# Performance work log

Hardware: AMD Instinct MI355X
Metric: run time of the kernel (lower is better)

Reference implementation:

```python
import jax, jax.numpy as jnp
import numpy as np

B, S, D, H, P = 4, 512, 4096, 32, 10
HD = D // H          # 128
R = 16               # lora rank
HID = 11008          # multiple_of-rounded 2/3 * 4*dim
MAXSEQ = 512
EPS = 1e-5
SCALE = 1.0 / (HD ** 0.5)


def setup_inputs() -> dict:
    key = jax.random.key(0)
    ks = jax.random.split(key, 40)
    rn = lambda k, shp, s=0.02: (jax.random.normal(k, shp, jnp.float32) * s)
    inp = {}
    inp['x'] = jax.random.normal(ks[0], (B, S, D), jnp.float32)
    inp['prompt'] = jax.random.normal(ks[1], (B, P, D), jnp.float32)
    causal = jnp.where(jnp.arange(S)[:, None] >= jnp.arange(S)[None, :], 0.0, -1e9)
    inp['mask'] = causal[None, None].astype(jnp.float32)
    inp['cache_k'] = jnp.zeros((B, MAXSEQ, H, HD), jnp.float32)
    inp['cache_v'] = jnp.zeros((B, MAXSEQ, H, HD), jnp.float32)
    freqs = 1.0 / (10000.0 ** (np.arange(0, HD, 2)[: HD // 2].astype(np.float32) / HD))
    ang = np.outer(np.arange(S), freqs).astype(np.float32)  # [S, HD//2]
    inp['freqs_cos'] = jnp.asarray(np.cos(ang))
    inp['freqs_sin'] = jnp.asarray(np.sin(ang))
    # attention weights (torch Linear layout: [out, in])
    inp['wq_w'] = rn(ks[2], (D, D)); inp['wq_b'] = jnp.zeros((D,), jnp.float32)
    inp['wk_w'] = rn(ks[3], (D, D))
    inp['wv_w'] = rn(ks[4], (D, D))
    inp['wo_w'] = rn(ks[5], (D, D)); inp['wo_b'] = jnp.zeros((D,), jnp.float32)
    inp['lq1'] = rn(ks[6], (R, D)); inp['lq2'] = rn(ks[7], (D, R), 0.01)
    inp['lk1'] = rn(ks[8], (R, D)); inp['lk2'] = rn(ks[9], (D, R), 0.01)
    inp['lv1'] = rn(ks[10], (R, D)); inp['lv2'] = rn(ks[11], (D, R), 0.01)
    inp['lo1'] = rn(ks[12], (R, D)); inp['lo2'] = rn(ks[13], (D, R), 0.01)
    inp['gate'] = rn(ks[14], (1, H, 1, 1), 0.5)
    inp['new_gate'] = jnp.ones((1, 1, 1, 1), jnp.float32)
    inp['attn_norm_w'] = jnp.ones((D,), jnp.float32)
    inp['ffn_norm_w'] = jnp.ones((D,), jnp.float32)
    inp['w1_w'] = rn(ks[15], (HID, D)); inp['w1_b'] = jnp.zeros((HID,), jnp.float32)
    inp['w2_w'] = rn(ks[16], (D, HID)); inp['w2_b'] = jnp.zeros((D,), jnp.float32)
    inp['w3_w'] = rn(ks[17], (HID, D)); inp['w3_b'] = jnp.zeros((HID,), jnp.float32)
    inp['fl1a'] = rn(ks[18], (R, D)); inp['fl1b'] = rn(ks[19], (HID, R), 0.01)
    inp['fl2a'] = rn(ks[20], (R, HID)); inp['fl2b'] = rn(ks[21], (D, R), 0.01)
    inp['fl3a'] = rn(ks[22], (R, D)); inp['fl3b'] = rn(ks[23], (HID, R), 0.01)
    inp['start_pos'] = 0
    return inp


def _rms(v, w):
    return v * jax.lax.rsqrt(jnp.mean(v * v, axis=-1, keepdims=True) + EPS) * w


def _rope(t, cos, sin):
    # t: [B,S,H,HD]; treat last dim as interleaved (real, imag) pairs
    t2 = t.reshape(*t.shape[:-1], HD // 2, 2)
    a, b = t2[..., 0], t2[..., 1]
    c = cos[None, :, None, :]
    s = sin[None, :, None, :]
    return jnp.stack([a * c - b * s, a * s + b * c], axis=-1).reshape(t.shape)


def reference(x, prompt, mask, cache_k, cache_v, freqs_cos, freqs_sin,
              wq_w, wq_b, wk_w, wv_w, wo_w, wo_b,
              lq1, lq2, lk1, lk2, lv1, lv2, lo1, lo2,
              gate, new_gate, attn_norm_w, ffn_norm_w,
              w1_w, w1_b, w2_w, w2_b, w3_w, w3_b,
              fl1a, fl1b, fl2a, fl2b, fl3a, fl3b, start_pos):
    bsz, seqlen, _ = x.shape
    # --- attention sub-layer ---
    h = _rms(x, attn_norm_w)
    xq = h @ wq_w.T + wq_b + (h @ lq1.T) @ lq2.T
    xk = h @ wk_w.T + (h @ lk1.T) @ lk2.T
    xv = h @ wv_w.T + (h @ lv1.T) @ lv2.T
    xq = xq.reshape(bsz, seqlen, H, HD)
    xk = xk.reshape(bsz, seqlen, H, HD)
    xv = xv.reshape(bsz, seqlen, H, HD)
    xq = _rope(xq, freqs_cos, freqs_sin)
    xk = _rope(xk, freqs_cos, freqs_sin)
    # KV-cache update (functional)
    cache_k = jax.lax.dynamic_update_slice(cache_k, xk, (0, start_pos, 0, 0))
    cache_v = jax.lax.dynamic_update_slice(cache_v, xv, (0, start_pos, 0, 0))
    keys = cache_k[:, : start_pos + seqlen].transpose(0, 2, 1, 3)    # b h k d
    values = cache_v[:, : start_pos + seqlen].transpose(0, 2, 1, 3)  # b h k d
    q = xq.transpose(0, 2, 1, 3)                                     # b h q d
    scores = jnp.einsum('bhqd,bhkd->bhqk', q, keys) * SCALE
    scores = jax.nn.softmax(scores + mask, axis=-1)
    out = jnp.einsum('bhqk,bhkd->bhqd', scores, values)
    # gated prompt attention branch (no LoRA on prompt k/v, matching source)
    pk = (prompt @ wk_w.T).reshape(bsz, P, H, HD).transpose(0, 2, 1, 3)
    pv = (prompt @ wv_w.T).reshape(bsz, P, H, HD).transpose(0, 2, 1, 3)
    ps = jnp.einsum('bhqd,bhpd->bhqp', q, pk) * SCALE
    ps = jnp.tanh(gate) * new_gate * jax.nn.softmax(ps, axis=-1)
    out = out + jnp.einsum('bhqp,bhpd->bhqd', ps, pv)
    out = out.transpose(0, 2, 1, 3).reshape(bsz, seqlen, D)
    attn = out @ wo_w.T + wo_b + (out @ lo1.T) @ lo2.T
    h2 = x + attn
    # --- SwiGLU FFN with LoRA ---
    g = _rms(h2, ffn_norm_w)
    a1 = g @ w1_w.T + w1_b + (g @ fl1a.T) @ fl1b.T
    a3 = g @ w3_w.T + w3_b + (g @ fl3a.T) @ fl3b.T
    o = jax.nn.silu(a1) * a3
    ffn = o @ w2_w.T + w2_b + (o @ fl2a.T) @ fl2b.T
    return h2 + ffn
```

## Files before the change

### kernel.cpp

```cpp
#include <hip/hip_runtime.h>

typedef int    i32x4 __attribute__((ext_vector_type(4)));
typedef float  f32x4 __attribute__((ext_vector_type(4)));
typedef __bf16 bf16x8 __attribute__((ext_vector_type(8)));
typedef unsigned int u32;
typedef unsigned short u16;

#define SCALEF 0.08838834764831845f
#define EPSF 1e-5f

__device__ __forceinline__ u16 f2bf(float f) {
  u32 u = __float_as_uint(f);
  u32 r = (u + 0x7fffu + ((u >> 16) & 1u)) >> 16;
  return (u16)r;
}
__device__ __forceinline__ float bf2f(u16 h) { return __uint_as_float(((u32)h) << 16); }
__device__ __forceinline__ u32 pack2(float a, float b) {
  return (u32)f2bf(a) | ((u32)f2bf(b) << 16);
}

__device__ __forceinline__ void gload16(const u16* g, u16* l) {
  __builtin_amdgcn_global_load_lds(
      (const __attribute__((address_space(1))) void*)g,
      (__attribute__((address_space(3))) void*)l, 16, 0, 0);
}


#define G_PHASE(MFMAS) \
  __builtin_amdgcn_s_barrier(); \
  __builtin_amdgcn_s_setprio(1); \
  MFMAS \
  __builtin_amdgcn_s_setprio(0); \
  __builtin_amdgcn_s_barrier();

#define MM(KH, MB, MI, NI) \
  acc[(MB)+(MI)][NI] = __builtin_amdgcn_mfma_f32_16x16x32_bf16( \
      aa[KH][MI], bb[KH][NI], acc[(MB)+(MI)][NI], 0, 0, 0);

#define MM8(MB, NI) MM(0,MB,0,NI) MM(0,MB,1,NI) MM(0,MB,2,NI) MM(0,MB,3,NI) \
                    MM(1,MB,0,NI) MM(1,MB,1,NI) MM(1,MB,2,NI) MM(1,MB,3,NI)

#define RDA4(P, KH, MG) \
  aa[KH][0] = *(const bf16x8*)(pAk[P][KH] + ((MG)*4+0)*2048); \
  aa[KH][1] = *(const bf16x8*)(pAk[P][KH] + ((MG)*4+1)*2048); \
  aa[KH][2] = *(const bf16x8*)(pAk[P][KH] + ((MG)*4+2)*2048); \
  aa[KH][3] = *(const bf16x8*)(pAk[P][KH] + ((MG)*4+3)*2048);

#define RDB1(P, NI) \
  bb[0][NI] = *(const bf16x8*)(pBk[P][0] + (NI)*2048); \
  bb[1][NI] = *(const bf16x8*)(pBk[P][1] + (NI)*2048);

#define STAGE_A(P, HH, KT) \
  gload16(sA + ((HH)*2+0)*lda64 + (long)(KT)*64, (u16*)(lds + (P)*BUFB + (HH)*16384 + w*1024)); \
  gload16(sA + ((HH)*2+1)*lda64 + (long)(KT)*64, (u16*)(lds + (P)*BUFB + (HH)*16384 + 8192 + w*1024));

#define STAGE_B(P, HH, KT) \
  gload16(sB + ((HH)*2+0)*ldb64 + (long)(KT)*64, (u16*)(lds + (P)*BUFB + 32768 + (HH)*16384 + w*1024)); \
  gload16(sB + ((HH)*2+1)*ldb64 + (long)(KT)*64, (u16*)(lds + (P)*BUFB + 32768 + (HH)*16384 + 8192 + w*1024));

#define GEMM_TILE(P, PN, TA, TC) \
  RDA4(P,0,0) RDA4(P,1,0) \
  RDB1(P,0) RDB1(P,1) \
  STAGE_A(PN, 1, TA) \
  G_PHASE(MM8(0,0) MM8(0,1)) \
  RDB1(P,2) RDB1(P,3) \
  G_PHASE(MM8(0,2) MM8(0,3)) \
  RDA4(P,0,1) RDA4(P,1,1) \
  STAGE_B(P, 0, TC) \
  G_PHASE(MM8(4,0) MM8(4,1)) \
  STAGE_B(P, 1, TC) \
  STAGE_A(P, 0, TC) \
  asm volatile("s_waitcnt vmcnt(6)" ::: "memory"); \
  G_PHASE(MM8(4,2) MM8(4,3))

#define GEMM_TILE2(P, PN, TA, TC) \
  RDA4(P,0,0) RDA4(P,1,0) \
  RDB1(P,0) RDB1(P,1) \
  STAGE_A(PN, 0, TA) \
  STAGE_A(PN, 1, TA) \
  G_PHASE(MM8(0,0) MM8(0,1)) \
  RDA4(P,0,1) RDA4(P,1,1) \
  STAGE_B(P, 0, TC) \
  asm volatile("s_waitcnt vmcnt(2)" ::: "memory"); \
  G_PHASE(MM8(4,0) MM8(4,1))

template<int NF, int OUT>
__global__ __launch_bounds__(512, 2) void gemm256(
    const u16* __restrict__ A, const u16* __restrict__ B, void* Cv,
    const float* __restrict__ bias, const float* __restrict__ bias2, int nsplit,
    const float* res, int K, int lda, int ldb, int ldc)
{
  extern __shared__ char lds[];
  constexpr int BN = NF * 64;
  constexpr int BUFB = (NF == 4) ? 65536 : 49152;

  const int tid = threadIdx.x, w = tid >> 6, l = tid & 63;
  const int wm = w >> 2, wn = w & 3;

  const int gy = gridDim.y;
  const int nwg = gridDim.x * gy;
  const int orig = blockIdx.y * gridDim.x + blockIdx.x;
  const int q = nwg >> 3, r = nwg & 7;
  const int xcd = orig & 7, sidx = orig >> 3;
  const int wg = (xcd < r ? xcd * (q + 1) : r * (q + 1) + (xcd - r) * q) + sidx;
  const int bx = wg / gy, by = wg % gy;
  const long row0 = (long)by * 256, col0 = (long)bx * BN;

  const int g4 = l >> 4, h8 = l & 7, r16 = l & 15;
  const int cs0 = ((g4 ^ h8) << 4);
  const int cs1 = cs0 ^ 64;
  const char* pAk[2][2];
  const char* pBk[2][2];
  {
    const int aoff = wm * 16384 + r16 * 128;
    const int boff = 32768 + ((NF == 4) ? ((wn >> 1) * 16384 + (wn & 1) * 8192)
                                        : (wn * 4096)) + r16 * 128;
    pAk[0][0] = lds + aoff + cs0;        pAk[0][1] = lds + aoff + cs1;
    pAk[1][0] = pAk[0][0] + BUFB;        pAk[1][1] = pAk[0][1] + BUFB;
    pBk[0][0] = lds + boff + cs0;        pBk[0][1] = lds + boff + cs1;
    pBk[1][0] = pBk[0][0] + BUFB;        pBk[1][1] = pBk[0][1] + BUFB;
  }

  const long ldaL = lda, ldbL = ldb;
  const long lda64 = ldaL * 64, ldb64 = ldbL * 64;
  const int srow = w * 8 + (l >> 3);
  const int scol = ((h8 ^ (l >> 3)) << 3);
  const u16* sA = A + (row0 + srow) * ldaL + scol;
  const u16* sB = B + (col0 + srow) * ldbL + scol;

  f32x4 acc[8][4];
  #pragma unroll
  for (int m = 0; m < 8; m++)
    #pragma unroll
    for (int n = 0; n < 4; n++)
      #pragma unroll
      for (int j = 0; j < 4; j++) acc[m][n][j] = 0.f;

  bf16x8 aa[2][4], bb[2][4];

  const int NT = K >> 6;
  if constexpr (NF == 4) {
    STAGE_A(0,0,0) STAGE_A(0,1,0) STAGE_B(0,0,0) STAGE_B(0,1,0)
    STAGE_B(1,0,1) STAGE_B(1,1,1) STAGE_A(1,0,1)
    asm volatile("s_waitcnt vmcnt(6)" ::: "memory");
    __builtin_amdgcn_s_barrier();
    for (int t = 0; t < NT; t += 2) {
      const int ta = (t + 1 < NT) ? t + 1 : NT - 1;
      const int tb = (t + 2 < NT) ? t + 2 : NT - 1;
      const int tc = (t + 3 < NT) ? t + 3 : NT - 1;
      GEMM_TILE(0, 1, ta, tb)
      GEMM_TILE(1, 0, tb, tc)
    }
  } else {
    STAGE_A(0,0,0) STAGE_A(0,1,0) STAGE_B(0,0,0)
    STAGE_B(1,0,1)
    asm volatile("s_waitcnt vmcnt(2)" ::: "memory");
    __builtin_amdgcn_s_barrier();
    for (int t = 0; t < NT; t += 2) {
      const int ta = (t + 1 < NT) ? t + 1 : NT - 1;
      const int tb = (t + 2 < NT) ? t + 2 : NT - 1;
      const int tc = (t + 3 < NT) ? t + 3 : NT - 1;
      GEMM_TILE2(0, 1, ta, tb)
      GEMM_TILE2(1, 0, tb, tc)
    }
  }

  const int cc = l & 15, cr = (l >> 4) * 4;
  #pragma unroll
  for (int mf = 0; mf < 8; mf++) {
    const long rrow = row0 + wm * 128 + mf * 16 + cr;
    if constexpr (OUT == 2) {
      #pragma unroll
      for (int nfp = 0; nfp < NF / 2; nfp++) {
        const long outc = (col0 >> 1) + wn * 32 + nfp * 16 + cc;
        const float b1 = bias[outc], b3 = bias2[outc];
        #pragma unroll
        for (int j = 0; j < 4; j++) {
          const float v1 = acc[mf][2 * nfp][j] + b1;
          const float v3 = acc[mf][2 * nfp + 1][j] + b3;
          const float o = v1 / (1.f + __expf(-v1)) * v3;
          ((u16*)Cv)[(rrow + j) * ldc + outc] = f2bf(o);
        }
      }
    } else {
      #pragma unroll
      for (int nf = 0; nf < 4 && nf < NF; nf++) {
        const long ccol = col0 + wn * (NF * 16) + nf * 16 + cc;
        float bb2 = 0.f;
        if (bias) bb2 = (ccol < nsplit) ? bias[ccol] : (bias2 ? bias2[ccol - nsplit] : 0.f);
        #pragma unroll
        for (int j = 0; j < 4; j++) {
          const long off = (rrow + j) * ldc + ccol;
          float v = acc[mf][nf][j] + bb2;
          if constexpr (OUT == 0) {
            if (res) v += res[off];
            ((float*)Cv)[off] = v;
          } else {
            ((u16*)Cv)[off] = f2bf(v);
          }
        }
      }
    }
  }
}

template<int EPI>
__global__ __launch_bounds__(256) void gemm_bt(
    const u16* __restrict__ A, const u16* __restrict__ B,
    float* __restrict__ Cf, u16* __restrict__ Cbf, const float* __restrict__ Cadd,
    int K, int lda, int ldb, int ldc, float scale,
    long sAb, long sBb, int cInnerN, long cSO, long cSI, int causal, int kvar)
{
  if (causal && blockIdx.x > blockIdx.y) return;
  const int Keff = kvar ? (int)(blockIdx.y + 1) * 128 : K;

  __shared__ u16 As[128*32] __attribute__((aligned(16)));
  __shared__ u16 Bs[128*32] __attribute__((aligned(16)));
  const int tid  = threadIdx.x;
  const int wave = tid >> 6, lane = tid & 63;
  const int wm = wave >> 1, wn = wave & 1;
  const int z = blockIdx.z;
  const u16* Ab = A + (long)z * sAb;
  const u16* Bb = B + (long)z * sBb;
  const long cb = (long)(z / cInnerN) * cSO + (long)(z % cInnerN) * cSI;

  const int sr = lane >> 2;
  const int sc = (lane & 3) * 8;
  const int c0 = wave * 2, c1 = wave * 2 + 1;
  const u16* gA0 = Ab + (long)(blockIdx.y * 128 + c0 * 16 + sr) * lda + sc;
  const u16* gA1 = Ab + (long)(blockIdx.y * 128 + c1 * 16 + sr) * lda + sc;
  const u16* gB0 = Bb + (long)(blockIdx.x * 128 + c0 * 16 + sr) * ldb + sc;
  const u16* gB1 = Bb + (long)(blockIdx.x * 128 + c1 * 16 + sr) * ldb + sc;
  u16* lA0 = &As[c0 * 512]; u16* lA1 = &As[c1 * 512];
  u16* lB0 = &Bs[c0 * 512]; u16* lB1 = &Bs[c1 * 512];

  f32x4 acc[4][4];
  #pragma unroll
  for (int m = 0; m < 4; m++)
    #pragma unroll
    for (int n = 0; n < 4; n++)
      #pragma unroll
      for (int j = 0; j < 4; j++) acc[m][n][j] = 0.f;

  const int fr  = lane & 15;
  const int fg8 = (lane >> 4) * 8;

  for (int k0 = 0; k0 < Keff; k0 += 32) {
    __syncthreads();
    gload16(gA0 + k0, lA0);
    gload16(gA1 + k0, lA1);
    gload16(gB0 + k0, lB0);
    gload16(gB1 + k0, lB1);
    __syncthreads();

    bf16x8 af[4], bfr[4];
    #pragma unroll
    for (int m = 0; m < 4; m++)
      af[m] = *(const bf16x8*)&As[(wm * 64 + m * 16 + fr) * 32 + fg8];
    #pragma unroll
    for (int n = 0; n < 4; n++)
      bfr[n] = *(const bf16x8*)&Bs[(wn * 64 + n * 16 + fr) * 32 + fg8];

    #pragma unroll
    for (int m = 0; m < 4; m++)
      #pragma unroll
      for (int n = 0; n < 4; n++)
        acc[m][n] = __builtin_amdgcn_mfma_f32_16x16x32_bf16(af[m], bfr[n], acc[m][n], 0, 0, 0);
  }

  const int cc = lane & 15, cr = (lane >> 4) * 4;
  #pragma unroll
  for (int m = 0; m < 4; m++) {
    const int row = blockIdx.y * 128 + wm * 64 + m * 16 + cr;
    #pragma unroll
    for (int n = 0; n < 4; n++) {
      const int col = blockIdx.x * 128 + wn * 64 + n * 16 + cc;
      #pragma unroll
      for (int j = 0; j < 4; j++) {
        const long off = cb + (long)(row + j) * ldc + col;
        const float v = acc[m][n][j] * scale;
        if constexpr (EPI == 0) Cf[off] = v;
        else                    Cbf[off] = f2bf(v + Cadd[off]);
      }
    }
  }
}

__device__ __forceinline__ void pack_rows4(const float* __restrict__ w,
    const float* __restrict__ l2, const float* __restrict__ l1,
    u16* __restrict__ out, long srcRow0, long outRow0, int K) {
  __shared__ float l2s[4][16];
  if (threadIdx.x < 64) l2s[threadIdx.x >> 4][threadIdx.x & 15] =
      l2[(srcRow0 + (threadIdx.x >> 4)) * 16 + (threadIdx.x & 15)];
  __syncthreads();
  const float s00 = l2s[0][0];
  (void)s00;
  for (int c = threadIdx.x * 4; c < K; c += 1024) {
    float4 v0 = *(const float4*)(w + (srcRow0 + 0) * K + c);
    float4 v1 = *(const float4*)(w + (srcRow0 + 1) * K + c);
    float4 v2 = *(const float4*)(w + (srcRow0 + 2) * K + c);
    float4 v3 = *(const float4*)(w + (srcRow0 + 3) * K + c);
    #pragma unroll 4
    for (int i = 0; i < 16; i++) {
      const float4 lv = *(const float4*)(l1 + (long)i * K + c);
      const float a0 = l2s[0][i], a1 = l2s[1][i], a2 = l2s[2][i], a3 = l2s[3][i];
      v0.x += a0 * lv.x; v0.y += a0 * lv.y; v0.z += a0 * lv.z; v0.w += a0 * lv.w;
      v1.x += a1 * lv.x; v1.y += a1 * lv.y; v1.z += a1 * lv.z; v1.w += a1 * lv.w;
      v2.x += a2 * lv.x; v2.y += a2 * lv.y; v2.z += a2 * lv.z; v2.w += a2 * lv.w;
      v3.x += a3 * lv.x; v3.y += a3 * lv.y; v3.z += a3 * lv.z; v3.w += a3 * lv.w;
    }
    uint2 p0, p1, p2, p3;
    p0.x = pack2(v0.x, v0.y); p0.y = pack2(v0.z, v0.w);
    p1.x = pack2(v1.x, v1.y); p1.y = pack2(v1.z, v1.w);
    p2.x = pack2(v2.x, v2.y); p2.y = pack2(v2.z, v2.w);
    p3.x = pack2(v3.x, v3.y); p3.y = pack2(v3.z, v3.w);
    *(uint2*)(out + (outRow0 + 0) * K + c) = p0;
    *(uint2*)(out + (outRow0 + 1) * K + c) = p1;
    *(uint2*)(out + (outRow0 + 2) * K + c) = p2;
    *(uint2*)(out + (outRow0 + 3) * K + c) = p3;
  }
}

__global__ __launch_bounds__(256) void pack4(
    const float* w0, const float* a0, const float* b0, u16* o0,
    const float* w1, const float* a1, const float* b1, u16* o1,
    const float* w2, const float* a2, const float* b2, u16* o2,
    const float* w3, const float* a3, const float* b3, u16* o3) {
  const int sel = blockIdx.x >> 10;
  const long row0 = (long)(blockIdx.x & 1023) * 4;
  const float* w;  const float* l2; const float* l1; u16* out;
  switch (sel) {
    case 0:  w = w0; l2 = a0; l1 = b0; out = o0; break;
    case 1:  w = w1; l2 = a1; l1 = b1; out = o1; break;
    case 2:  w = w2; l2 = a2; l1 = b2; out = o2; break;
    default: w = w3; l2 = a3; l1 = b3; out = o3; break;
  }
  pack_rows4(w, l2, l1, out, row0, row0, 4096);
}

__global__ __launch_bounds__(256) void packw4(const float* __restrict__ w,
    const float* __restrict__ l2, const float* __restrict__ l1,
    u16* __restrict__ out, int K) {
  const long row0 = (long)blockIdx.x * 4;
  pack_rows4(w, l2, l1, out, row0, row0, K);
}

__global__ __launch_bounds__(256) void packw13_4(const float* __restrict__ w1,
    const float* __restrict__ l2_1, const float* __restrict__ l1_1,
    const float* __restrict__ w3,
    const float* __restrict__ l2_3, const float* __restrict__ l1_3,
    u16* __restrict__ out) {
  const long row0 = (long)blockIdx.x * 4;
  const int s = ((int)row0 >> 4) & 1;
  const long src0 = (row0 >> 5) * 16 + (row0 & 15);
  pack_rows4(s ? w3 : w1, s ? l2_3 : l2_1, s ? l1_3 : l1_1, out, src0, row0, 4096);
}

__global__ __launch_bounds__(256) void prep(const float* __restrict__ x, const float* __restrict__ w,
                                            const float* __restrict__ prompt, u16* __restrict__ out) {
  const int bid = blockIdx.x;
  if (bid < 2048) {
    const float4* xr = (const float4*)(x + (long)bid * 4096);
    const float4* wr = (const float4*)w;
    float4 v[4];
    float ss = 0.f;
    #pragma unroll
    for (int j = 0; j < 4; j++) {
      v[j] = xr[threadIdx.x + j * 256];
      ss += v[j].x * v[j].x + v[j].y * v[j].y + v[j].z * v[j].z + v[j].w * v[j].w;
    }
    #pragma unroll
    for (int off = 32; off; off >>= 1) ss += __shfl_xor(ss, off);
    __shared__ float wsum[4];
    if ((threadIdx.x & 63) == 0) wsum[threadIdx.x >> 6] = ss;
    __syncthreads();
    const float sc = rsqrtf((wsum[0] + wsum[1] + wsum[2] + wsum[3]) * (1.f / 4096.f) + EPSF);
    u16* orow = out + (long)bid * 4096;
    #pragma unroll
    for (int j = 0; j < 4; j++) {
      float4 wv = wr[threadIdx.x + j * 256];
      int idx = (threadIdx.x + j * 256) * 4;
      uint2 p;
      p.x = pack2(v[j].x * sc * wv.x, v[j].y * sc * wv.y);
      p.y = pack2(v[j].z * sc * wv.z, v[j].w * sc * wv.w);
      *(uint2*)&orow[idx] = p;
    }
  } else if (bid < 2088) {
    const int r = bid - 2048;
    const float4* src = (const float4*)(prompt + (long)r * 4096);
    u16* dst = out + (long)(2048 + r) * 4096;
    #pragma unroll
    for (int j = 0; j < 4; j++) {
      float4 v = src[threadIdx.x + j * 256];
      int idx = (threadIdx.x + j * 256) * 4;
      uint2 p; p.x = pack2(v.x, v.y); p.y = pack2(v.z, v.w);
      *(uint2*)&dst[idx] = p;
    }
  } else {
    u16* dst = out + (long)bid * 4096 + threadIdx.x * 16;
    i32x4 z; z[0] = 0; z[1] = 0; z[2] = 0; z[3] = 0;
    *(i32x4*)dst = z;
    *(i32x4*)(dst + 8) = z;
  }
}

__global__ __launch_bounds__(256) void lorap(const u16* __restrict__ Ap,
    const float* __restrict__ L1k, const float* __restrict__ L2k,
    const float* __restrict__ L1v, const float* __restrict__ L2v,
    u16* __restrict__ xqkv) {
  const int row = blockIdx.x;
  const int lane = threadIdx.x & 63, wave = threadIdx.x >> 6;
  __shared__ float tk[16], tv[16];
  const u16* a = Ap + (long)row * 4096;
  {
    const float* k0 = L1k + (long)(wave * 4 + 0) * 4096;
    const float* k1 = L1k + (long)(wave * 4 + 1) * 4096;
    const float* k2 = L1k + (long)(wave * 4 + 2) * 4096;
    const float* k3 = L1k + (long)(wave * 4 + 3) * 4096;
    const float* v0 = L1v + (long)(wave * 4 + 0) * 4096;
    const float* v1 = L1v + (long)(wave * 4 + 1) * 4096;
    const float* v2 = L1v + (long)(wave * 4 + 2) * 4096;
    const float* v3 = L1v + (long)(wave * 4 + 3) * 4096;
    float ak0 = 0, ak1 = 0, ak2 = 0, ak3 = 0;
    float av0 = 0, av1 = 0, av2 = 0, av3 = 0;
    for (int k = lane; k < 4096; k += 64) {
      const float av = bf2f(a[k]);
      ak0 += av * k0[k]; ak1 += av * k1[k]; ak2 += av * k2[k]; ak3 += av * k3[k];
      av0 += av * v0[k]; av1 += av * v1[k]; av2 += av * v2[k]; av3 += av * v3[k];
    }
    #pragma unroll
    for (int off = 32; off; off >>= 1) {
      ak0 += __shfl_down(ak0, off); ak1 += __shfl_down(ak1, off);
      ak2 += __shfl_down(ak2, off); ak3 += __shfl_down(ak3, off);
      av0 += __shfl_down(av0, off); av1 += __shfl_down(av1, off);
      av2 += __shfl_down(av2, off); av3 += __shfl_down(av3, off);
    }
    if (lane == 0) {
      tk[wave * 4 + 0] = ak0; tk[wave * 4 + 1] = ak1;
      tk[wave * 4 + 2] = ak2; tk[wave * 4 + 3] = ak3;
      tv[wave * 4 + 0] = av0; tv[wave * 4 + 1] = av1;
      tv[wave * 4 + 2] = av2; tv[wave * 4 + 3] = av3;
    }
  }
  __syncthreads();
  u16* xr = xqkv + (long)(2048 + row) * 12288;
  for (int col = threadIdx.x; col < 4096; col += 256) {
    float addk = 0.f, addv = 0.f;
    const float* lk = L2k + (long)col * 16;
    const float* lv = L2v + (long)col * 16;
    #pragma unroll
    for (int r = 0; r < 16; r++) { addk += tk[r] * lk[r]; addv += tv[r] * lv[r]; }
    xr[4096 + col] = f2bf(bf2f(xr[4096 + col]) - addk);
    xr[8192 + col] = f2bf(bf2f(xr[8192 + col]) - addv);
  }
}

__global__ __launch_bounds__(256) void layout(const u16* __restrict__ xqkv,
    const float* __restrict__ cosT, const float* __restrict__ sinT,
    u16* __restrict__ qbf, u16* __restrict__ kbf, u16* __restrict__ vt,
    u16* __restrict__ pk, u16* __restrict__ pv) {
  const int bid = blockIdx.x;
  if (bid < 2048) {
    const int s = bid & 511, b = bid >> 9;
    for (int pp = threadIdx.x; pp < 2048; pp += 256) {
      const int h = pp >> 6, ip = pp & 63;
      const float c = cosT[s * 64 + ip], sn = sinT[s * 64 + ip];
      const long src = (long)bid * 12288 + h * 128 + ip * 2;
      const u32 qv = *(const u32*)(xqkv + src);
      const u32 kv = *(const u32*)(xqkv + src + 4096);
      const float qx = bf2f((u16)qv), qy = bf2f((u16)(qv >> 16));
      const float kx = bf2f((u16)kv), ky = bf2f((u16)(kv >> 16));
      const long dst = ((long)(b * 32 + h) * 512 + s) * 128 + ip * 2;
      *(u32*)&qbf[dst] = pack2(qx * c - qy * sn, qx * sn + qy * c);
      *(u32*)&kbf[dst] = pack2(kx * c - ky * sn, kx * sn + ky * c);
    }
  } else if (bid < 10240) {
    const int idx = bid - 2048;
    const int s0 = (idx & 15) * 32, d0 = ((idx >> 4) & 3) * 32, bh = idx >> 6;
    const int b = bh >> 5, h = bh & 31;
    __shared__ u16 tile[32][33];
    const int tx = threadIdx.x & 31, ty = threadIdx.x >> 5;
    #pragma unroll
    for (int j = 0; j < 4; j++) {
      const int s = s0 + ty + j * 8;
      tile[ty + j * 8][tx] = xqkv[(long)(b * 512 + s) * 12288 + 8192 + h * 128 + d0 + tx];
    }
    __syncthreads();
    #pragma unroll
    for (int j = 0; j < 4; j++) {
      const int d = d0 + ty + j * 8;
      vt[((long)bh * 128 + d) * 512 + s0 + tx] = tile[tx][ty + j * 8];
    }
  } else {
    const int rp = bid - 10240;
    const int b = rp / 10, p = rp % 10;
    const u16* src = xqkv + (long)(2048 + rp) * 12288;
    for (int col = threadIdx.x * 2; col < 4096; col += 512) {
      const int h = col >> 7, d = col & 127;
      const long dst = ((long)(b * 32 + h) * 10 + p) * 128 + d;
      *(u32*)&pk[dst] = *(const u32*)&src[4096 + col];
      *(u32*)&pv[dst] = *(const u32*)&src[8192 + col];
    }
  }
}

__global__ __launch_bounds__(256) void smpa(const float* __restrict__ sc, u16* __restrict__ P,
    const u16* __restrict__ qbf, const u16* __restrict__ pk, const u16* __restrict__ pv,
    const float* __restrict__ gate, const float* __restrict__ ngate, float* __restrict__ attnp) {
  const int bid = blockIdx.x;
  const int lane = threadIdx.x & 63;
  if (bid < 16384) {
    const int r = bid * 4 + (threadIdx.x >> 6);
    const int q = r & 511;
    const float* srow = sc + (long)r * 512 + lane * 8;
    float v[8]; float m = -3e38f;
    #pragma unroll
    for (int j = 0; j < 8; j++) {
      const int col = lane * 8 + j;
      v[j] = (col <= q) ? srow[j] : -3e38f;
      m = fmaxf(m, v[j]);
    }
    #pragma unroll
    for (int off = 32; off; off >>= 1) m = fmaxf(m, __shfl_xor(m, off));
    float sum = 0.f;
    #pragma unroll
    for (int j = 0; j < 8; j++) { v[j] = __expf(v[j] - m); sum += v[j]; }
    #pragma unroll
    for (int off = 32; off; off >>= 1) sum += __shfl_xor(sum, off);
    const float inv = 1.f / sum;
    i32x4 o;
    o[0] = (int)pack2(v[0] * inv, v[1] * inv); o[1] = (int)pack2(v[2] * inv, v[3] * inv);
    o[2] = (int)pack2(v[4] * inv, v[5] * inv); o[3] = (int)pack2(v[6] * inv, v[7] * inv);
    *(i32x4*)(P + (long)r * 512 + lane * 8) = o;
  } else {
    const int r = (bid - 16384) * 4 + (threadIdx.x >> 6);
    const int bh = r >> 9, q = r & 511, b = bh >> 5, h = bh & 31;
    const u32 qraw = *(const u32*)&qbf[(long)r * 128 + lane * 2];
    const float q0 = bf2f((u16)qraw), q1 = bf2f((u16)(qraw >> 16));
    float s[10];
    #pragma unroll
    for (int p = 0; p < 10; p++) {
      const u32 kraw = *(const u32*)&pk[((long)bh * 10 + p) * 128 + lane * 2];
      float d = q0 * bf2f((u16)kraw) + q1 * bf2f((u16)(kraw >> 16));
      #pragma unroll
      for (int off = 32; off; off >>= 1) d += __shfl_xor(d, off);
      s[p] = d * SCALEF;
    }
    float m = s[0];
    #pragma unroll
    for (int p = 1; p < 10; p++) m = fmaxf(m, s[p]);
    float sum = 0.f;
    #pragma unroll
    for (int p = 0; p < 10; p++) { s[p] = __expf(s[p] - m); sum += s[p]; }
    const float gt = tanhf(gate[h]) * ngate[0] / sum;
    float o0 = 0.f, o1 = 0.f;
    #pragma unroll
    for (int p = 0; p < 10; p++) {
      const u32 vraw = *(const u32*)&pv[((long)bh * 10 + p) * 128 + lane * 2];
      o0 += s[p] * bf2f((u16)vraw); o1 += s[p] * bf2f((u16)(vraw >> 16));
    }
    float2 ov = make_float2(gt * o0, gt * o1);
    *(float2*)&attnp[(long)(b * 512 + q) * 4096 + h * 128 + lane * 2] = ov;
  }
}

extern "C" void kernel_launch(void* const* d_in, const int* in_sizes, int n_in,
                              void* d_out, int out_size, void* d_ws, size_t ws_size,
                              hipStream_t stream) {
  const float* x      = (const float*)d_in[0];
  const float* prompt = (const float*)d_in[1];
  const float* fcos   = (const float*)d_in[5];
  const float* fsin   = (const float*)d_in[6];
  const float* wq     = (const float*)d_in[7];
  const float* wq_b   = (const float*)d_in[8];
  const float* wk     = (const float*)d_in[9];
  const float* wv     = (const float*)d_in[10];
  const float* wo     = (const float*)d_in[11];
  const float* wo_b   = (const float*)d_in[12];
  const float* lq1    = (const float*)d_in[13];
  const float* lq2    = (const float*)d_in[14];
  const float* lk1    = (const float*)d_in[15];
  const float* lk2    = (const float*)d_in[16];
  const float* lv1    = (const float*)d_in[17];
  const float* lv2    = (const float*)d_in[18];
  const float* lo1    = (const float*)d_in[19];
  const float* lo2    = (const float*)d_in[20];
  const float* gate   = (const float*)d_in[21];
  const float* ngate  = (const float*)d_in[22];
  const float* anw    = (const float*)d_in[23];
  const float* fnw    = (const float*)d_in[24];
  const float* w1     = (const float*)d_in[25];
  const float* w1_b   = (const float*)d_in[26];
  const float* w2     = (const float*)d_in[27];
  const float* w2_b   = (const float*)d_in[28];
  const float* w3     = (const float*)d_in[29];
  const float* w3_b   = (const float*)d_in[30];
  const float* fl1a   = (const float*)d_in[31];
  const float* fl1b   = (const float*)d_in[32];
  const float* fl2a   = (const float*)d_in[33];
  const float* fl2b   = (const float*)d_in[34];
  const float* fl3a   = (const float*)d_in[35];
  const float* fl3b   = (const float*)d_in[36];
  float* out = (float*)d_out;

  char* base = (char*)d_ws;
  u16* Wq  = (u16*)(base + 0L);
  u16* Wo  = (u16*)(base + 100663296L);
  u16* W13 = (u16*)(base + 134217728L);
  u16* W2  = (u16*)(base + 314572800L);
  u16* Abf = (u16*)(base + 404750336L);
  const long SP = 423624704L;
  u16*   xqkv    = (u16*)(base + SP);
  float* scoresB = (float*)(base + SP);
  u16*   obf     = (u16*)(base + SP);
  u16*   qbf     = (u16*)(base + SP + 134217728L);
  u16*   kbf     = (u16*)(base + SP + 150994944L);
  u16*   vt      = (u16*)(base + SP + 167772160L);
  u16*   pk      = (u16*)(base + SP + 184549376L);
  u16*   pv      = (u16*)(base + SP + 184877056L);
  u16*   Pbf     = (u16*)(base + SP + 185204736L);
  float* attnp   = (float*)(base + SP + 252313600L);
  u16*   attnbf  = (u16*)(base + SP + 285868032L);
  u16*   gbf     = (u16*)(base + SP + 302645248L);
  const long TOTAL = SP + 319422464L + 131072L;
  if ((long)ws_size < TOTAL) return;

  dim3 blk(256);
  {
    auto f41 = gemm256<4, 1>; auto f42 = gemm256<4, 2>; auto f2 = gemm256<2, 0>;
    (void)hipFuncSetAttribute((const void*)f41, hipFuncAttributeMaxDynamicSharedMemorySize, 131072);
    (void)hipFuncSetAttribute((const void*)f42, hipFuncAttributeMaxDynamicSharedMemorySize, 131072);
    (void)hipFuncSetAttribute((const void*)f2,  hipFuncAttributeMaxDynamicSharedMemorySize, 98304);
  }

  pack4<<<4096, blk, 0, stream>>>(wq, lq2, lq1, Wq,
                                  wk, lk2, lk1, Wq + 16777216L,
                                  wv, lv2, lv1, Wq + 33554432L,
                                  wo, lo2, lo1, Wo);
  packw13_4<<<5504, blk, 0, stream>>>(w1, fl1b, fl1a, w3, fl3b, fl3a, W13);
  packw4<<<1024, blk, 0, stream>>>(w2, fl2b, fl2a, W2, 11008);

  prep<<<2304, blk, 0, stream>>>(x, anw, prompt, Abf);

  gemm256<4, 1><<<dim3(48, 9), 512, 131072, stream>>>(Abf, Wq, xqkv, wq_b, nullptr, 4096,
      nullptr, 4096, 4096, 4096, 12288);
  lorap<<<40, blk, 0, stream>>>(Abf + 2048L * 4096, lk1, lk2, lv1, lv2, xqkv);

  layout<<<10280, blk, 0, stream>>>(xqkv, fcos, fsin, qbf, kbf, vt, pk, pv);

  gemm_bt<0><<<dim3(4, 4, 128), blk, 0, stream>>>(qbf, kbf, scoresB, nullptr, nullptr,
      128, 128, 128, 512, SCALEF, 65536L, 65536L, 1, 262144L, 0, 1, 0);
  smpa<<<32768, blk, 0, stream>>>(scoresB, Pbf, qbf, pk, pv, gate, ngate, attnp);
  gemm_bt<1><<<dim3(1, 4, 128), blk, 0, stream>>>(Pbf, vt, nullptr, attnbf, attnp,
      512, 512, 512, 4096, 1.f, 262144L, 65536L, 32, 2097152L, 128L, 0, 1);

  gemm256<2, 0><<<dim3(32, 8), 512, 98304, stream>>>(attnbf, Wo, out, wo_b, nullptr, 1 << 30,
      x, 4096, 4096, 4096, 4096);

  prep<<<2048, blk, 0, stream>>>(out, fnw, nullptr, gbf);
  gemm256<4, 2><<<dim3(86, 8), 512, 131072, stream>>>(gbf, W13, obf, w1_b, w3_b, 0,
      nullptr, 4096, 4096, 4096, 11008);
  gemm256<2, 0><<<dim3(32, 8), 512, 98304, stream>>>(obf, W2, out, w2_b, nullptr, 1 << 30,
      out, 11008, 11008, 11008, 4096);
}
```

Measured before the change: 1.405 ms.

## Fuse RoPE and head-major scatter into QKV GEMM epilogue, bf16 scores

```diff
diff --git a/kernel.cpp b/kernel.cpp
--- a/kernel.cpp
+++ b/kernel.cpp
@@ -88,7 +88,9 @@
 __global__ __launch_bounds__(512, 2) void gemm256(
     const u16* __restrict__ A, const u16* __restrict__ B, void* Cv,
     const float* __restrict__ bias, const float* __restrict__ bias2, int nsplit,
-    const float* res, int K, int lda, int ldb, int ldc)
+    const float* res, int K, int lda, int ldb, int ldc,
+    u16* __restrict__ kout, u16* __restrict__ vout, u16* __restrict__ pout,
+    const float* __restrict__ fcos, const float* __restrict__ fsin)
 {
   extern __shared__ char lds[];
   constexpr int BN = NF * 64;
@@ -105,6 +107,10 @@
   const int wg = (xcd < r ? xcd * (q + 1) : r * (q + 1) + (xcd - r) * q) + sidx;
   const int bx = wg / gy, by = wg % gy;
   const long row0 = (long)by * 256, col0 = (long)bx * BN;
+
+  if constexpr (OUT == 3) {
+    if (col0 < 4096 && row0 >= 2048) return;
+  }
 
   const int g4 = l >> 4, h8 = l & 7, r16 = l & 15;
   const int cs0 = ((g4 ^ h8) << 4);
@@ -166,37 +172,76 @@
   }
 
   const int cc = l & 15, cr = (l >> 4) * 4;
-  #pragma unroll
-  for (int mf = 0; mf < 8; mf++) {
-    const long rrow = row0 + wm * 128 + mf * 16 + cr;
-    if constexpr (OUT == 2) {
+  if constexpr (OUT == 3) {
+    const int reg = (int)(col0 >> 12);
+    const bool isP = (row0 >= 2048);
+    #pragma unroll
+    for (int mf = 0; mf < 8; mf++) {
+      const long rrow = row0 + wm * 128 + mf * 16 + cr;
       #pragma unroll
-      for (int nfp = 0; nfp < NF / 2; nfp++) {
-        const long outc = (col0 >> 1) + wn * 32 + nfp * 16 + cc;
-        const float b1 = bias[outc], b3 = bias2[outc];
+      for (int nf = 0; nf < 4; nf++) {
+        const long ccol = col0 + wn * 64 + nf * 16 + cc;
         #pragma unroll
         for (int j = 0; j < 4; j++) {
-          const float v1 = acc[mf][2 * nfp][j] + b1;
-          const float v3 = acc[mf][2 * nfp + 1][j] + b3;
-          const float o = v1 / (1.f + __expf(-v1)) * v3;
-          ((u16*)Cv)[(rrow + j) * ldc + outc] = f2bf(o);
+          float v = acc[mf][nf][j];
+          const long grow = rrow + j;
+          if (reg == 0) {
+            v += bias[ccol];
+            const int s = (int)(grow & 511), bb_ = (int)(grow >> 9);
+            const int d = (int)(ccol & 127), h = (int)((ccol >> 7) & 31);
+            const int ip = d >> 1;
+            const float c = fcos[s * 64 + ip], sn = fsin[s * 64 + ip];
+            const float other = __shfl_xor(v, 1);
+            const float rr = (d & 1) ? (other * sn + v * c) : (v * c - other * sn);
+            ((u16*)Cv)[((long)(bb_ * 32 + h) * 512 + s) * 128 + d] = f2bf(rr);
+          } else if (reg == 1) {
+            if (!isP) {
+              const int s = (int)(grow & 511), bb_ = (int)(grow >> 9);
+              const int d = (int)(ccol & 127), h = (int)((ccol >> 7) & 31);
+              const int ip = d >> 1;
+              const float c = fcos[s * 64 + ip], sn = fsin[s * 64 + ip];
+              const float other = __shfl_xor(v, 1);
+              const float rr = (d & 1) ? (other * sn + v * c) : (v * c - other * sn);
+              kout[((long)(bb_ * 32 + h) * 512 + s) * 128 + d] = f2bf(rr);
+            } else {
+              pout[(grow - 2048) * 8192 + (ccol - 4096)] = f2bf(v);
+            }
+          } else {
+            if (!isP) vout[grow * 4096 + (ccol - 8192)] = f2bf(v);
+            else      pout[(grow - 2048) * 8192 + 4096 + (ccol - 8192)] = f2bf(v);
+          }
         }
       }
-    } else {
-      #pragma unroll
-      for (int nf = 0; nf < 4 && nf < NF; nf++) {
-        const long ccol = col0 + wn * (NF * 16) + nf * 16 + cc;
-        float bb2 = 0.f;
-        if (bias) bb2 = (ccol < nsplit) ? bias[ccol] : (bias2 ? bias2[ccol - nsplit] : 0.f);
+    }
+  } else {
+    #pragma unroll
+    for (int mf = 0; mf < 8; mf++) {
+      const long rrow = row0 + wm * 128 + mf * 16 + cr;
+      if constexpr (OUT == 2) {
         #pragma unroll
-        for (int j = 0; j < 4; j++) {
-          const long off = (rrow + j) * ldc + ccol;
-          float v = acc[mf][nf][j] + bb2;
-          if constexpr (OUT == 0) {
+        for (int nfp = 0; nfp < NF / 2; nfp++) {
+          const long outc = (col0 >> 1) + wn * 32 + nfp * 16 + cc;
+          const float b1 = bias[outc], b3 = bias2[outc];
+          #pragma unroll
+          for (int j = 0; j < 4; j++) {
+            const float v1 = acc[mf][2 * nfp][j] + b1;
+            const float v3 = acc[mf][2 * nfp + 1][j] + b3;
+            const float o = v1 / (1.f + __expf(-v1)) * v3;
+            ((u16*)Cv)[(rrow + j) * ldc + outc] = f2bf(o);
+          }
+        }
+      } else {
+        #pragma unroll
+        for (int nf = 0; nf < 4 && nf < NF; nf++) {
+          const long ccol = col0 + wn * (NF * 16) + nf * 16 + cc;
+          float bb2 = 0.f;
+          if (bias) bb2 = (ccol < nsplit) ? bias[ccol] : (bias2 ? bias2[ccol - nsplit] : 0.f);
+          #pragma unroll
+          for (int j = 0; j < 4; j++) {
+            const long off = (rrow + j) * ldc + ccol;
+            float v = acc[mf][nf][j] + bb2;
             if (res) v += res[off];
             ((float*)Cv)[off] = v;
-          } else {
-            ((u16*)Cv)[off] = f2bf(v);
           }
         }
       }
@@ -279,8 +324,9 @@
       for (int j = 0; j < 4; j++) {
         const long off = cb + (long)(row + j) * ldc + col;
         const float v = acc[m][n][j] * scale;
-        if constexpr (EPI == 0) Cf[off] = v;
-        else                    Cbf[off] = f2bf(v + Cadd[off]);
+        if constexpr (EPI == 0)      Cf[off] = v;
+        else if constexpr (EPI == 1) Cbf[off] = f2bf(v + Cadd[off]);
+        else                         Cbf[off] = f2bf(v);
       }
     }
   }
@@ -293,8 +339,6 @@
   if (threadIdx.x < 64) l2s[threadIdx.x >> 4][threadIdx.x & 15] =
       l2[(srcRow0 + (threadIdx.x >> 4)) * 16 + (threadIdx.x & 15)];
   __syncthreads();
-  const float s00 = l2s[0][0];
-  (void)s00;
   for (int c = threadIdx.x * 4; c < K; c += 1024) {
     float4 v0 = *(const float4*)(w + (srcRow0 + 0) * K + c);
     float4 v1 = *(const float4*)(w + (srcRow0 + 1) * K + c);
@@ -407,7 +451,7 @@
 __global__ __launch_bounds__(256) void lorap(const u16* __restrict__ Ap,
     const float* __restrict__ L1k, const float* __restrict__ L2k,
     const float* __restrict__ L1v, const float* __restrict__ L2v,
-    u16* __restrict__ xqkv) {
+    u16* __restrict__ pbuf) {
   const int row = blockIdx.x;
   const int lane = threadIdx.x & 63, wave = threadIdx.x >> 6;
   __shared__ float tk[16], tv[16];
@@ -443,47 +487,30 @@
     }
   }
   __syncthreads();
-  u16* xr = xqkv + (long)(2048 + row) * 12288;
+  u16* pr = pbuf + (long)row * 8192;
   for (int col = threadIdx.x; col < 4096; col += 256) {
     float addk = 0.f, addv = 0.f;
     const float* lk = L2k + (long)col * 16;
     const float* lv = L2v + (long)col * 16;
     #pragma unroll
     for (int r = 0; r < 16; r++) { addk += tk[r] * lk[r]; addv += tv[r] * lv[r]; }
-    xr[4096 + col] = f2bf(bf2f(xr[4096 + col]) - addk);
-    xr[8192 + col] = f2bf(bf2f(xr[8192 + col]) - addv);
-  }
-}
-
-__global__ __launch_bounds__(256) void layout(const u16* __restrict__ xqkv,
-    const float* __restrict__ cosT, const float* __restrict__ sinT,
-    u16* __restrict__ qbf, u16* __restrict__ kbf, u16* __restrict__ vt,
-    u16* __restrict__ pk, u16* __restrict__ pv) {
+    pr[col] = f2bf(bf2f(pr[col]) - addk);
+    pr[4096 + col] = f2bf(bf2f(pr[4096 + col]) - addv);
+  }
+}
+
+__global__ __launch_bounds__(256) void layout(const u16* __restrict__ vbuf, const u16* __restrict__ pbuf,
+    u16* __restrict__ vt, u16* __restrict__ pk, u16* __restrict__ pv) {
   const int bid = blockIdx.x;
-  if (bid < 2048) {
-    const int s = bid & 511, b = bid >> 9;
-    for (int pp = threadIdx.x; pp < 2048; pp += 256) {
-      const int h = pp >> 6, ip = pp & 63;
-      const float c = cosT[s * 64 + ip], sn = sinT[s * 64 + ip];
-      const long src = (long)bid * 12288 + h * 128 + ip * 2;
-      const u32 qv = *(const u32*)(xqkv + src);
-      const u32 kv = *(const u32*)(xqkv + src + 4096);
-      const float qx = bf2f((u16)qv), qy = bf2f((u16)(qv >> 16));
-      const float kx = bf2f((u16)kv), ky = bf2f((u16)(kv >> 16));
-      const long dst = ((long)(b * 32 + h) * 512 + s) * 128 + ip * 2;
-      *(u32*)&qbf[dst] = pack2(qx * c - qy * sn, qx * sn + qy * c);
-      *(u32*)&kbf[dst] = pack2(kx * c - ky * sn, kx * sn + ky * c);
-    }
-  } else if (bid < 10240) {
-    const int idx = bid - 2048;
-    const int s0 = (idx & 15) * 32, d0 = ((idx >> 4) & 3) * 32, bh = idx >> 6;
+  if (bid < 8192) {
+    const int s0 = (bid & 15) * 32, d0 = ((bid >> 4) & 3) * 32, bh = bid >> 6;
     const int b = bh >> 5, h = bh & 31;
     __shared__ u16 tile[32][33];
     const int tx = threadIdx.x & 31, ty = threadIdx.x >> 5;
     #pragma unroll
     for (int j = 0; j < 4; j++) {
       const int s = s0 + ty + j * 8;
-      tile[ty + j * 8][tx] = xqkv[(long)(b * 512 + s) * 12288 + 8192 + h * 128 + d0 + tx];
+      tile[ty + j * 8][tx] = vbuf[(long)(b * 512 + s) * 4096 + h * 128 + d0 + tx];
     }
     __syncthreads();
     #pragma unroll
@@ -492,19 +519,19 @@
       vt[((long)bh * 128 + d) * 512 + s0 + tx] = tile[tx][ty + j * 8];
     }
   } else {
-    const int rp = bid - 10240;
+    const int rp = bid - 8192;
     const int b = rp / 10, p = rp % 10;
-    const u16* src = xqkv + (long)(2048 + rp) * 12288;
+    const u16* src = pbuf + (long)rp * 8192;
     for (int col = threadIdx.x * 2; col < 4096; col += 512) {
       const int h = col >> 7, d = col & 127;
       const long dst = ((long)(b * 32 + h) * 10 + p) * 128 + d;
-      *(u32*)&pk[dst] = *(const u32*)&src[4096 + col];
-      *(u32*)&pv[dst] = *(const u32*)&src[8192 + col];
-    }
-  }
-}
-
-__global__ __launch_bounds__(256) void smpa(const float* __restrict__ sc, u16* __restrict__ P,
+      *(u32*)&pk[dst] = *(const u32*)&src[col];
+      *(u32*)&pv[dst] = *(const u32*)&src[4096 + col];
+    }
+  }
+}
+
+__global__ __launch_bounds__(256) void smpa(const u16* __restrict__ sc, u16* __restrict__ P,
     const u16* __restrict__ qbf, const u16* __restrict__ pk, const u16* __restrict__ pv,
     const float* __restrict__ gate, const float* __restrict__ ngate, float* __restrict__ attnp) {
   const int bid = blockIdx.x;
@@ -512,12 +539,15 @@
   if (bid < 16384) {
     const int r = bid * 4 + (threadIdx.x >> 6);
     const int q = r & 511;
-    const float* srow = sc + (long)r * 512 + lane * 8;
+    const u16* srow = sc + (long)r * 512 + lane * 8;
+    i32x4 raw = *(const i32x4*)srow;
     float v[8]; float m = -3e38f;
     #pragma unroll
     for (int j = 0; j < 8; j++) {
+      const u32 u = (u32)raw[j >> 1];
+      const float val = bf2f((j & 1) ? (u16)(u >> 16) : (u16)u);
       const int col = lane * 8 + j;
-      v[j] = (col <= q) ? srow[j] : -3e38f;
+      v[j] = (col <= q) ? val : -3e38f;
       m = fmaxf(m, v[j]);
     }
     #pragma unroll
@@ -610,25 +640,26 @@
   u16* W2  = (u16*)(base + 314572800L);
   u16* Abf = (u16*)(base + 404750336L);
   const long SP = 423624704L;
-  u16*   xqkv    = (u16*)(base + SP);
-  float* scoresB = (float*)(base + SP);
-  u16*   obf     = (u16*)(base + SP);
-  u16*   qbf     = (u16*)(base + SP + 134217728L);
-  u16*   kbf     = (u16*)(base + SP + 150994944L);
-  u16*   vt      = (u16*)(base + SP + 167772160L);
-  u16*   pk      = (u16*)(base + SP + 184549376L);
-  u16*   pv      = (u16*)(base + SP + 184877056L);
-  u16*   Pbf     = (u16*)(base + SP + 185204736L);
-  float* attnp   = (float*)(base + SP + 252313600L);
-  u16*   attnbf  = (u16*)(base + SP + 285868032L);
-  u16*   gbf     = (u16*)(base + SP + 302645248L);
+  u16*   scores16 = (u16*)(base + SP);
+  u16*   obf      = (u16*)(base + SP);
+  u16*   vbuf     = (u16*)(base + SP + 73400320L);
+  u16*   pbuf     = (u16*)(base + SP + 92274688L);
+  u16*   qbf      = (u16*)(base + SP + 134217728L);
+  u16*   kbf      = (u16*)(base + SP + 150994944L);
+  u16*   vt       = (u16*)(base + SP + 167772160L);
+  u16*   pk       = (u16*)(base + SP + 184549376L);
+  u16*   pv       = (u16*)(base + SP + 184877056L);
+  u16*   Pbf      = (u16*)(base + SP + 185204736L);
+  float* attnp    = (float*)(base + SP + 252313600L);
+  u16*   attnbf   = (u16*)(base + SP + 285868032L);
+  u16*   gbf      = (u16*)(base + SP + 302645248L);
   const long TOTAL = SP + 319422464L + 131072L;
   if ((long)ws_size < TOTAL) return;
 
   dim3 blk(256);
   {
-    auto f41 = gemm256<4, 1>; auto f42 = gemm256<4, 2>; auto f2 = gemm256<2, 0>;
-    (void)hipFuncSetAttribute((const void*)f41, hipFuncAttributeMaxDynamicSharedMemorySize, 131072);
+    auto f43 = gemm256<4, 3>; auto f42 = gemm256<4, 2>; auto f2 = gemm256<2, 0>;
+    (void)hipFuncSetAttribute((const void*)f43, hipFuncAttributeMaxDynamicSharedMemorySize, 131072);
     (void)hipFuncSetAttribute((const void*)f42, hipFuncAttributeMaxDynamicSharedMemorySize, 131072);
     (void)hipFuncSetAttribute((const void*)f2,  hipFuncAttributeMaxDynamicSharedMemorySize, 98304);
   }
@@ -642,24 +673,24 @@
 
   prep<<<2304, blk, 0, stream>>>(x, anw, prompt, Abf);
 
-  gemm256<4, 1><<<dim3(48, 9), 512, 131072, stream>>>(Abf, Wq, xqkv, wq_b, nullptr, 4096,
-      nullptr, 4096, 4096, 4096, 12288);
-  lorap<<<40, blk, 0, stream>>>(Abf + 2048L * 4096, lk1, lk2, lv1, lv2, xqkv);
-
-  layout<<<10280, blk, 0, stream>>>(xqkv, fcos, fsin, qbf, kbf, vt, pk, pv);
-
-  gemm_bt<0><<<dim3(4, 4, 128), blk, 0, stream>>>(qbf, kbf, scoresB, nullptr, nullptr,
+  gemm256<4, 3><<<dim3(48, 9), 512, 131072, stream>>>(Abf, Wq, qbf, wq_b, nullptr, 0,
+      nullptr, 4096, 4096, 4096, 0, kbf, vbuf, pbuf, fcos, fsin);
+  lorap<<<40, blk, 0, stream>>>(Abf + 2048L * 4096, lk1, lk2, lv1, lv2, pbuf);
+
+  layout<<<8232, blk, 0, stream>>>(vbuf, pbuf, vt, pk, pv);
+
+  gemm_bt<2><<<dim3(4, 4, 128), blk, 0, stream>>>(qbf, kbf, nullptr, scores16, nullptr,
       128, 128, 128, 512, SCALEF, 65536L, 65536L, 1, 262144L, 0, 1, 0);
-  smpa<<<32768, blk, 0, stream>>>(scoresB, Pbf, qbf, pk, pv, gate, ngate, attnp);
+  smpa<<<32768, blk, 0, stream>>>(scores16, Pbf, qbf, pk, pv, gate, ngate, attnp);
   gemm_bt<1><<<dim3(1, 4, 128), blk, 0, stream>>>(Pbf, vt, nullptr, attnbf, attnp,
       512, 512, 512, 4096, 1.f, 262144L, 65536L, 32, 2097152L, 128L, 0, 1);
 
   gemm256<2, 0><<<dim3(32, 8), 512, 98304, stream>>>(attnbf, Wo, out, wo_b, nullptr, 1 << 30,
-      x, 4096, 4096, 4096, 4096);
+      x, 4096, 4096, 4096, 4096, nullptr, nullptr, nullptr, nullptr, nullptr);
 
   prep<<<2048, blk, 0, stream>>>(out, fnw, nullptr, gbf);
   gemm256<4, 2><<<dim3(86, 8), 512, 131072, stream>>>(gbf, W13, obf, w1_b, w3_b, 0,
-      nullptr, 4096, 4096, 4096, 11008);
+      nullptr, 4096, 4096, 4096, 11008, nullptr, nullptr, nullptr, nullptr, nullptr);
   gemm256<2, 0><<<dim3(32, 8), 512, 98304, stream>>>(obf, W2, out, w2_b, nullptr, 1 << 30,
-      out, 11008, 11008, 11008, 4096);
-}
+      out, 11008, 11008, 11008, 4096, nullptr, nullptr, nullptr, nullptr, nullptr);
+}
```

Measured after the change: 1.429 ms. Within noise of the previous version (+1.7%).
